# Optimization experiments

Hardware: AMD Instinct MI355X
Metric: run time of the kernel (lower is better)

Reference implementation:

```python
import jax, jax.numpy as jnp
import numpy as np

HIDDEN = 4096
NUM_HEADS = 32
NUM_KV_HEADS = 8
HEAD_DIM = 128
ROPE_THETA = 10000.0


def setup_inputs() -> dict:
    key = jax.random.key(0)
    ks = jax.random.split(key, 5)
    B, N = 2, 2048
    s = 0.02
    return {
        "hidden_states": jax.random.normal(ks[0], (B, N, HIDDEN), dtype=jnp.float32),
        "positions": jnp.tile(jnp.arange(N, dtype=jnp.int32)[None, :], (B, 1)),
        "Wq": jax.random.normal(ks[1], (HIDDEN, NUM_HEADS * HEAD_DIM), dtype=jnp.float32) * s,
        "Wk": jax.random.normal(ks[2], (HIDDEN, NUM_KV_HEADS * HEAD_DIM), dtype=jnp.float32) * s,
        "Wv": jax.random.normal(ks[3], (HIDDEN, NUM_KV_HEADS * HEAD_DIM), dtype=jnp.float32) * s,
        "Wo": jax.random.normal(ks[4], (NUM_HEADS * HEAD_DIM, HIDDEN), dtype=jnp.float32) * s,
    }


def _rotate_half(x):
    half = x.shape[-1] // 2
    return jnp.concatenate([-x[..., half:], x[..., :half]], axis=-1)


def reference(hidden_states, positions, Wq, Wk, Wv, Wo):
    B, N, _ = hidden_states.shape
    H, KVH, D = NUM_HEADS, NUM_KV_HEADS, HEAD_DIM
    rep = H // KVH

    # projections
    q = (hidden_states @ Wq).reshape(B, N, H, D).transpose(0, 2, 1, 3)     # [B,H,N,D]
    k = (hidden_states @ Wk).reshape(B, N, KVH, D).transpose(0, 2, 1, 3)   # [B,KVH,N,D]
    v = (hidden_states @ Wv).reshape(B, N, KVH, D).transpose(0, 2, 1, 3)   # [B,KVH,N,D]

    # rotary embedding
    inv_freq = 1.0 / (ROPE_THETA ** (jnp.arange(0, D, 2, dtype=jnp.float32) / D))
    freqs = positions.astype(jnp.float32)[..., None] * inv_freq            # [B,N,D/2]
    emb = jnp.concatenate([freqs, freqs], axis=-1)                          # [B,N,D]
    cos = jnp.cos(emb)[:, None, :, :]                                       # [B,1,N,D]
    sin = jnp.sin(emb)[:, None, :, :]
    q = q * cos + _rotate_half(q) * sin
    k = k * cos + _rotate_half(k) * sin

    # GQA attention without materializing repeated k/v:
    # group q heads by kv head (repeat_interleave => q head h uses kv group h//rep)
    qg = q.reshape(B, KVH, rep, N, D)
    scale = 1.0 / jnp.sqrt(jnp.asarray(D, dtype=q.dtype))
    scores = jnp.einsum('bgrnd,bgmd->bgrnm', qg, k) * scale                 # [B,KVH,rep,N,N]
    causal = jnp.tril(jnp.ones((N, N), dtype=bool))
    scores = jnp.where(causal, scores, jnp.finfo(scores.dtype).min)
    attn = jax.nn.softmax(scores, axis=-1)
    out = jnp.einsum('bgrnm,bgmd->bgrnd', attn, v)                          # [B,KVH,rep,N,D]
    out = out.reshape(B, H, N, D).transpose(0, 2, 1, 3).reshape(B, N, H * D)
    return out @ Wo
```

## Files before the change

### kernel.cpp

```cpp
#include <hip/hip_runtime.h>
#include <hip/hip_bf16.h>

typedef __bf16 bf16_t;
typedef float  f32x4  __attribute__((ext_vector_type(4)));
typedef bf16_t bf16x2 __attribute__((ext_vector_type(2)));
typedef bf16_t bf16x4 __attribute__((ext_vector_type(4)));
typedef bf16_t bf16x8 __attribute__((ext_vector_type(8)));

#define MFMA16(a, b, c) __builtin_amdgcn_mfma_f32_16x16x32_bf16((a), (b), (c), 0, 0, 0)

#define GLOAD_LDS16(g, l)                                                              \
  __builtin_amdgcn_global_load_lds((const __attribute__((address_space(1))) void*)(g), \
                                   (__attribute__((address_space(3))) void*)(l), 16, 0, 0)

#define BARRIER    __builtin_amdgcn_s_barrier()
#define WAIT_LGKM0 asm volatile("s_waitcnt lgkmcnt(0)" ::: "memory")
#define WAIT_LGKM8 asm volatile("s_waitcnt lgkmcnt(8)" ::: "memory")
#define WAIT_VM3   asm volatile("s_waitcnt vmcnt(3)" ::: "memory")
#define WAIT_VM4   asm volatile("s_waitcnt vmcnt(4)" ::: "memory")
#define WAIT_VM0   asm volatile("s_waitcnt vmcnt(0)" ::: "memory")

__global__ __launch_bounds__(256) void cvt_bf16(const float* __restrict__ in,
                                                bf16_t* __restrict__ out, int n4) {
  int stride = gridDim.x * blockDim.x;
  for (int i = blockIdx.x * blockDim.x + threadIdx.x; i < n4; i += stride) {
    f32x4 v = ((const f32x4*)in)[i];
    bf16x4 o;
#pragma unroll
    for (int j = 0; j < 4; ++j) o[j] = (bf16_t)v[j];
    ((bf16x4*)out)[i] = o;
  }
}

__global__ __launch_bounds__(256) void transpose_cvt(const float* __restrict__ in,
                                                     bf16_t* __restrict__ out,
                                                     int R, int C) {
  __shared__ float t[64][65];
  int tr0 = blockIdx.y * 64, tc0 = blockIdx.x * 64;
  int tx = threadIdx.x & 15, ty = threadIdx.x >> 4;
#pragma unroll
  for (int i = 0; i < 4; ++i) {
    f32x4 v = *(const f32x4*)(in + (size_t)(tr0 + ty + 16 * i) * C + tc0 + tx * 4);
#pragma unroll
    for (int j = 0; j < 4; ++j) t[ty + 16 * i][tx * 4 + j] = v[j];
  }
  __syncthreads();
#pragma unroll
  for (int i = 0; i < 4; ++i) {
    bf16x4 o4;
#pragma unroll
    for (int j = 0; j < 4; ++j) o4[j] = (bf16_t)t[tx * 4 + j][ty + 16 * i];
    *(bf16x4*)(out + (size_t)(tc0 + ty + 16 * i) * R + tr0 + tx * 4) = o4;
  }
}

#define LDB8(bf)                                                                         \
  {                                                                                      \
    const int sb_ = bBase0 + (bf)*16384;                                                 \
    _Pragma("unroll") for (int nf = 0; nf < 4; ++nf) {                                   \
      int row_ = brow0 + nf * 16 + ci;                                                   \
      _Pragma("unroll") for (int ks = 0; ks < 2; ++ks)                                   \
          b[nf][ks] = *(const bf16x8*)&lds[sb_ + row_ * 64 + ((ks * 32 + g * 8) ^ co)];  \
    }                                                                                    \
  }

#define LDA4(bf, q)                                                                      \
  {                                                                                      \
    const int sb_ = aBase0 + (bf)*16384;                                                 \
    _Pragma("unroll") for (int j = 0; j < 2; ++j) {                                      \
      int row_ = ((q)*2 + j) * 16 + ci;                                                  \
      _Pragma("unroll") for (int ks = 0; ks < 2; ++ks)                                   \
          a[j][ks] = *(const bf16x8*)&lds[sb_ + row_ * 64 + ((ks * 32 + g * 8) ^ co)];   \
    }                                                                                    \
  }

#define MMQ(q)                                                                           \
  {                                                                                      \
    __builtin_amdgcn_s_setprio(1);                                                       \
    _Pragma("unroll") for (int j = 0; j < 2; ++j)                                        \
        _Pragma("unroll") for (int nf = 0; nf < 4; ++nf)                                 \
            _Pragma("unroll") for (int ks = 0; ks < 2; ++ks)                             \
                acc[(q)*2 + j][nf] = MFMA16(a[j][ks], b[nf][ks], acc[(q)*2 + j][nf]);    \
    __builtin_amdgcn_s_setprio(0);                                                       \
  }

template <int WRITE_BF16>
__global__ __launch_bounds__(512) void gemm8o(const bf16_t* __restrict__ A,
                                              const bf16_t* __restrict__ Bt,
                                              void* __restrict__ Cv,
                                              int N, int K, int ntn) {
  __shared__ alignas(16) bf16_t lds[65536];
  const int tid = threadIdx.x;
  const int lane = tid & 63, w = tid >> 6;
  const int wr = w >> 2, wc = w & 3;
  const int g = lane >> 4, ci = lane & 15;
  const int cpx = gridDim.x >> 3;
  const int wg = ((int)blockIdx.x & 7) * cpx + ((int)blockIdx.x >> 3);
  const int m0 = (wg / ntn) * 256, n0 = (wg % ntn) * 256;
  const int ksw = ((lane & 7) ^ (lane >> 3)) << 3;
  const int aBase0 = wr * 8192;
  const int bBase0 = 32768 + (wc >> 1) * 8192;
  const int brow0 = (wc & 1) * 64;
  const int co = (ci & 7) << 3;

  const bf16_t* As[2] = {A + (size_t)m0 * K, A + (size_t)(m0 + 128) * K};
  const bf16_t* Bs[2] = {Bt + (size_t)n0 * K, Bt + (size_t)(n0 + 128) * K};

  auto stage = [&](const bf16_t* src, int kk, int ldsbase) {
#pragma unroll
    for (int j = 0; j < 2; ++j)
      GLOAD_LDS16(src + (size_t)(j * 64 + w * 8 + (lane >> 3)) * K + kk + ksw,
                  (char*)&lds[ldsbase + (j * 64 + w * 8) * 64]);
  };

  bf16x8 a[2][2], b[4][2];
  f32x4 acc[8][4];
#pragma unroll
  for (int mf = 0; mf < 8; ++mf)
#pragma unroll
    for (int nf = 0; nf < 4; ++nf) acc[mf][nf] = f32x4{0.f, 0.f, 0.f, 0.f};

  stage(As[0], 0, 0);
  stage(As[1], 0, 8192);
  stage(Bs[0], 0, 32768);
  stage(Bs[1], 0, 40960);
  stage(Bs[0], 64, 49152);
  stage(Bs[1], 64, 57344);
  WAIT_VM4;
  BARRIER;

  const int NT2 = K >> 7;
  for (int i = 0; i < NT2; ++i) {
    const int keb = i << 7;
    const int kA1 = keb + 64;
    int e2 = keb + 128;
    if (e2 > K - 64) e2 = K - 64;
    int o2 = keb + 192;
    if (o2 > K - 64) o2 = K - 64;
    LDA4(0, 0) LDB8(0)
    stage(As[0], kA1, 16384);
    WAIT_LGKM8;
    BARRIER; WAIT_LGKM0;
    MMQ(0)
    BARRIER;
    LDA4(0, 1)
    stage(As[1], kA1, 24576);
    BARRIER; WAIT_LGKM0;
    MMQ(1)
    BARRIER;
    LDA4(0, 2)
    stage(Bs[0], e2, 32768);
    BARRIER; WAIT_LGKM0;
    MMQ(2)
    BARRIER;
    LDA4(0, 3)
    stage(Bs[1], e2, 40960);
    BARRIER; WAIT_LGKM0;
    MMQ(3)
    WAIT_VM4;
    BARRIER;
    LDA4(1, 0) LDB8(1)
    stage(As[0], e2, 0);
    WAIT_LGKM8;
    BARRIER; WAIT_LGKM0;
    MMQ(0)
    BARRIER;
    LDA4(1, 1)
    stage(As[1], e2, 8192);
    BARRIER; WAIT_LGKM0;
    MMQ(1)
    BARRIER;
    LDA4(1, 2)
    stage(Bs[0], o2, 49152);
    BARRIER; WAIT_LGKM0;
    MMQ(2)
    BARRIER;
    LDA4(1, 3)
    stage(Bs[1], o2, 57344);
    BARRIER; WAIT_LGKM0;
    MMQ(3)
    WAIT_VM4;
    BARRIER;
  }
  WAIT_VM0;

#pragma unroll
  for (int mf = 0; mf < 8; ++mf) {
#pragma unroll
    for (int nf = 0; nf < 4; ++nf) {
      int grow = m0 + wr * 128 + mf * 16 + g * 4;
      int gcol = n0 + wc * 64 + nf * 16 + ci;
#pragma unroll
      for (int r = 0; r < 4; ++r) {
        if (WRITE_BF16)
          ((bf16_t*)Cv)[(size_t)(grow + r) * N + gcol] = (bf16_t)acc[mf][nf][r];
        else
          ((float*)Cv)[(size_t)(grow + r) * N + gcol] = acc[mf][nf][r];
      }
    }
  }
}

#define QLDB12(bf)                                                                        \
  {                                                                                       \
    const int sb_ = 32768 + (bf)*12288;                                                   \
    _Pragma("unroll") for (int nf = 0; nf < 6; ++nf) {                                    \
      int row_ = wc * 96 + nf * 16 + ci;                                                  \
      _Pragma("unroll") for (int ks = 0; ks < 2; ++ks)                                    \
          b[nf][ks] = *(const bf16x8*)&lds[sb_ + row_ * 64 + ((ks * 32 + g * 8) ^ co)];   \
    }                                                                                     \
  }

#define QLDA2(bf, q)                                                                      \
  {                                                                                       \
    const int sb_ = (bf)*16384;                                                           \
    const int row_ = wr * 64 + (q)*16 + ci;                                               \
    _Pragma("unroll") for (int ks = 0; ks < 2; ++ks)                                      \
        a[ks] = *(const bf16x8*)&lds[sb_ + row_ * 64 + ((ks * 32 + g * 8) ^ co)];         \
  }

#define QMMQ(q)                                                                           \
  {                                                                                       \
    __builtin_amdgcn_s_setprio(1);                                                        \
    _Pragma("unroll") for (int nf = 0; nf < 6; ++nf)                                      \
        _Pragma("unroll") for (int ks = 0; ks < 2; ++ks)                                  \
            acc[q][nf] = MFMA16(a[ks], b[nf][ks], acc[q][nf]);                            \
    __builtin_amdgcn_s_setprio(0);                                                        \
  }

__global__ __launch_bounds__(512) void gemm8qkv(const bf16_t* __restrict__ A,
                                                const bf16_t* __restrict__ Bt,
                                                bf16_t* __restrict__ C,
                                                int N, int K, int ntn) {
  __shared__ alignas(16) bf16_t lds[57344];
  const int tid = threadIdx.x;
  const int lane = tid & 63, w = tid >> 6;
  const int wr = w >> 1, wc = w & 1;
  const int g = lane >> 4, ci = lane & 15;
  const int cpx = gridDim.x >> 3;
  const int wg = ((int)blockIdx.x & 7) * cpx + ((int)blockIdx.x >> 3);
  const int m0 = (wg / ntn) * 256, n0 = (wg % ntn) * 192;
  const int ksw = ((lane & 7) ^ (lane >> 3)) << 3;
  const int co = (ci & 7) << 3;

  const bf16_t* Ar[4] = {A + (size_t)m0 * K, A + (size_t)(m0 + 64) * K,
                         A + (size_t)(m0 + 128) * K, A + (size_t)(m0 + 192) * K};
  const bf16_t* Br[3] = {Bt + (size_t)n0 * K, Bt + (size_t)(n0 + 64) * K,
                         Bt + (size_t)(n0 + 128) * K};

  auto stage64 = [&](const bf16_t* src, int kk, int ldsbase) {
    GLOAD_LDS16(src + (size_t)(w * 8 + (lane >> 3)) * K + kk + ksw,
                (char*)&lds[ldsbase + w * 512]);
  };

  bf16x8 a[2], b[6][2];
  f32x4 acc[4][6];
#pragma unroll
  for (int mf = 0; mf < 4; ++mf)
#pragma unroll
    for (int nf = 0; nf < 6; ++nf) acc[mf][nf] = f32x4{0.f, 0.f, 0.f, 0.f};

#pragma unroll
  for (int c = 0; c < 4; ++c) stage64(Ar[c], 0, c * 4096);
#pragma unroll
  for (int c = 0; c < 3; ++c) stage64(Br[c], 0, 32768 + c * 4096);
#pragma unroll
  for (int c = 0; c < 3; ++c) stage64(Br[c], 64, 45056 + c * 4096);
  WAIT_VM3;
  BARRIER;

  const int NT2 = K >> 7;
  for (int i = 0; i < NT2; ++i) {
    const int keb = i << 7;
    const int kA1 = keb + 64;
    int e2 = keb + 128;
    if (e2 > K - 64) e2 = K - 64;
    int o2 = keb + 192;
    if (o2 > K - 64) o2 = K - 64;
    QLDA2(0, 0) QLDB12(0)
    stage64(Ar[0], kA1, 16384);
    stage64(Ar[1], kA1, 16384 + 4096);
    WAIT_LGKM8;
    BARRIER; WAIT_LGKM0;
    QMMQ(0)
    BARRIER;
    QLDA2(0, 1)
    stage64(Ar[2], kA1, 16384 + 8192);
    stage64(Ar[3], kA1, 16384 + 12288);
    BARRIER; WAIT_LGKM0;
    QMMQ(1)
    BARRIER;
    QLDA2(0, 2)
    stage64(Br[0], e2, 32768);
    stage64(Br[1], e2, 32768 + 4096);
    BARRIER; WAIT_LGKM0;
    QMMQ(2)
    BARRIER;
    QLDA2(0, 3)
    stage64(Br[2], e2, 32768 + 8192);
    BARRIER; WAIT_LGKM0;
    QMMQ(3)
    WAIT_VM3;
    BARRIER;
    QLDA2(1, 0) QLDB12(1)
    stage64(Ar[0], e2, 0);
    stage64(Ar[1], e2, 4096);
    WAIT_LGKM8;
    BARRIER; WAIT_LGKM0;
    QMMQ(0)
    BARRIER;
    QLDA2(1, 1)
    stage64(Ar[2], e2, 8192);
    stage64(Ar[3], e2, 12288);
    BARRIER; WAIT_LGKM0;
    QMMQ(1)
    BARRIER;
    QLDA2(1, 2)
    stage64(Br[0], o2, 45056);
    stage64(Br[1], o2, 45056 + 4096);
    BARRIER; WAIT_LGKM0;
    QMMQ(2)
    BARRIER;
    QLDA2(1, 3)
    stage64(Br[2], o2, 45056 + 8192);
    BARRIER; WAIT_LGKM0;
    QMMQ(3)
    WAIT_VM3;
    BARRIER;
  }
  WAIT_VM0;

#pragma unroll
  for (int mf = 0; mf < 4; ++mf) {
#pragma unroll
    for (int nf = 0; nf < 6; ++nf) {
      int grow = m0 + wr * 64 + mf * 16 + g * 4;
      int gcol = n0 + wc * 96 + nf * 16 + ci;
#pragma unroll
      for (int r = 0; r < 4; ++r)
        C[(size_t)(grow + r) * N + gcol] = (bf16_t)acc[mf][nf][r];
    }
  }
}

__global__ __launch_bounds__(256) void rope_kv(const bf16_t* __restrict__ QKV,
                                               const int* __restrict__ pos,
                                               bf16_t* __restrict__ Kr,
                                               bf16_t* __restrict__ Vr) {
  int unit = blockIdx.x * 8 + (threadIdx.x >> 5);
  int l = threadIdx.x & 31;
  int token = unit >> 3, kvh = unit & 7;
  int b = token >> 11, n = token & 2047;
  const bf16_t* base = QKV + (size_t)token * 6144;
  {
    const bf16_t* src = base + 4096 + kvh * 128;
    bf16_t* dst = Kr + ((size_t)(b * 8 + kvh) * 2048 + n) * 128;
    float p = (float)pos[token];
    float a0 = p * exp2f(-(float)(2 * l) * 0.20762050593045702f);
    float a1 = p * exp2f(-(float)(2 * l + 1) * 0.20762050593045702f);
    float sn0, cs0, sn1, cs1;
    sincosf(a0, &sn0, &cs0);
    sincosf(a1, &sn1, &cs1);
    bf16x2 x0 = *(const bf16x2*)(src + 2 * l);
    bf16x2 x1 = *(const bf16x2*)(src + 64 + 2 * l);
    bf16x2 o0, o1;
    o0[0] = (bf16_t)((float)x0[0] * cs0 - (float)x1[0] * sn0);
    o0[1] = (bf16_t)((float)x0[1] * cs1 - (float)x1[1] * sn1);
    o1[0] = (bf16_t)((float)x1[0] * cs0 + (float)x0[0] * sn0);
    o1[1] = (bf16_t)((float)x1[1] * cs1 + (float)x0[1] * sn1);
    *(bf16x2*)(dst + 2 * l) = o0;
    *(bf16x2*)(dst + 64 + 2 * l) = o1;
  }
  {
    const bf16_t* src = base + 5120 + kvh * 128;
    bf16_t* dst = Vr + ((size_t)(b * 8 + kvh) * 2048 + n) * 128;
    *(bf16x4*)(dst + 4 * l) = *(const bf16x4*)(src + 4 * l);
  }
}

__global__ __launch_bounds__(512) void attn_kernel(const bf16_t* __restrict__ QKV,
                                                   const bf16_t* __restrict__ K,
                                                   const bf16_t* __restrict__ V,
                                                   const int* __restrict__ pos,
                                                   bf16_t* __restrict__ O) {
  const float scale2 = 0.12751743f;
  __shared__ alignas(16) bf16_t Kl[64 * 128];
  __shared__ alignas(16) bf16_t Vt[128 * 64];
  __shared__ alignas(16) bf16_t Pl[8][32 * 64];
  const int tid = threadIdx.x;
  const int lane = tid & 63, w = tid >> 6;
  const int g = lane >> 4, ci = lane & 15;
  const int hb = blockIdx.y;
  const int b = hb >> 5, h = hb & 31, kvh = h >> 2;
  const int p = blockIdx.x;
  const int qtB = 15 - p;
  const int qr[2] = {p * 128 + w * 16, qtB * 128 + w * 16};
  const bf16_t* Kh = K + (size_t)(b * 8 + kvh) * 2048 * 128;
  const bf16_t* Vh = V + (size_t)(b * 8 + kvh) * 2048 * 128;

  bf16x8 bq[2][4];
#pragma unroll
  for (int qb = 0; qb < 2; ++qb) {
    const int n = qr[qb] + ci;
    const bf16_t* qp = QKV + (size_t)(b * 2048 + n) * 6144 + h * 128;
    bf16x8 raw[4];
#pragma unroll
    for (int ks = 0; ks < 4; ++ks) raw[ks] = *(const bf16x8*)(qp + ks * 32 + g * 8);
    float ppos = (float)pos[b * 2048 + n];
#pragma unroll
    for (int k2 = 0; k2 < 2; ++k2)
#pragma unroll
      for (int j = 0; j < 8; ++j) {
        int d = k2 * 32 + g * 8 + j;
        float ang = ppos * exp2f(-(float)d * 0.20762050593045702f);
        float sn, cs;
        sincosf(ang, &sn, &cs);
        float x0 = (float)raw[k2][j], x1 = (float)raw[k2 + 2][j];
        bq[qb][k2][j] = (bf16_t)(x0 * cs - x1 * sn);
        bq[qb][k2 + 2][j] = (bf16_t)(x1 * cs + x0 * sn);
      }
  }

  f32x4 o[2][8];
#pragma unroll
  for (int qb = 0; qb < 2; ++qb)
#pragma unroll
    for (int nb = 0; nb < 8; ++nb) o[qb][nb] = f32x4{0.f, 0.f, 0.f, 0.f};
  float mrow[2] = {-1e30f, -1e30f};
  float lrow[2] = {0.f, 0.f};

  bf16x8 kreg[2];
  bf16x4 rv[4];
  const int kq = tid >> 5, dq = tid & 31;
  auto loadKV = [&](int kv0) {
#pragma unroll
    for (int i = 0; i < 2; ++i) {
      int c = tid + i * 512;
      kreg[i] = *(const bf16x8*)(Kh + (size_t)(kv0 + (c >> 4)) * 128 + (c & 15) * 8);
    }
#pragma unroll
    for (int rr = 0; rr < 4; ++rr)
      rv[rr] = *(const bf16x4*)(Vh + (size_t)(kv0 + kq * 4 + rr) * 128 + dq * 4);
  };
  auto writeKV = [&]() {
#pragma unroll
    for (int i = 0; i < 2; ++i) {
      int c = tid + i * 512;
      int row = c >> 4, kc = (c & 15) * 8;
      int sw = ((row ^ (row >> 3)) & 7) << 4;
      *(bf16x8*)((char*)Kl + row * 256 + ((kc * 2) ^ sw)) = kreg[i];
    }
#pragma unroll
    for (int jj = 0; jj < 4; ++jj) {
      int d = dq * 4 + jj;
      bf16x4 cv;
#pragma unroll
      for (int rr = 0; rr < 4; ++rr) cv[rr] = rv[rr][jj];
      int sw = ((d ^ (d >> 3)) & 7) << 4;
      *(bf16x4*)((char*)Vt + d * 128 + ((kq * 8) ^ sw)) = cv;
    }
  };

  const int nt = (qtB + 1) * 2;
  loadKV(0);
  for (int t = 0; t < nt; ++t) {
    const int kv0 = t * 64;
    __syncthreads();
    writeKV();
    __syncthreads();
    if (t + 1 < nt) loadKV(kv0 + 64);

    bool act[2] = {kv0 <= qr[0] + 15, kv0 <= qr[1] + 15};
#pragma unroll
    for (int qb = 0; qb < 2; ++qb) {
      if (!act[qb]) continue;
      f32x4 st[4];
#pragma unroll
      for (int kvb = 0; kvb < 4; ++kvb) st[kvb] = f32x4{0.f, 0.f, 0.f, 0.f};
      __builtin_amdgcn_s_setprio(1);
#pragma unroll
      for (int kvb = 0; kvb < 4; ++kvb) {
        int row = kvb * 16 + ci;
        int sw = ((row ^ (row >> 3)) & 7) << 4;
#pragma unroll
        for (int ks = 0; ks < 4; ++ks) {
          bf16x8 ak = *(const bf16x8*)((char*)Kl + row * 256 + ((ks * 64 + g * 16) ^ sw));
          st[kvb] = MFMA16(ak, bq[qb][ks], st[kvb]);
        }
      }
      __builtin_amdgcn_s_setprio(0);
      const int q = qr[qb] + ci;
      const bool needmask = (kv0 + 63 > qr[qb]);
      float pv[16];
      float pm = -1e30f;
#pragma unroll
      for (int kvb = 0; kvb < 4; ++kvb)
#pragma unroll
        for (int r = 0; r < 4; ++r) {
          float v = st[kvb][r] * scale2;
          if (needmask && (kv0 + kvb * 16 + 4 * g + r > q)) v = -1e30f;
          pv[kvb * 4 + r] = v;
          pm = fmaxf(pm, v);
        }
      pm = fmaxf(pm, __shfl_xor(pm, 16));
      pm = fmaxf(pm, __shfl_xor(pm, 32));
      const bool nskip = !__all((int)(pm <= mrow[qb] + 11.5f));
      const float mold = mrow[qb];
      float mnew = mold;
      float fs = 1.0f;
      if (nskip) {
        mnew = fmaxf(mold, pm);
        fs = exp2f(mold - mnew);
        mrow[qb] = mnew;
      }
      float ps = 0.f;
#pragma unroll
      for (int e = 0; e < 16; ++e) {
        pv[e] = exp2f(pv[e] - mnew);
        ps += pv[e];
      }
      ps += __shfl_xor(ps, 16);
      ps += __shfl_xor(ps, 32);
      lrow[qb] = (nskip ? lrow[qb] * fs : lrow[qb]) + ps;
      int prow = qb * 16 + ci;
      int swp = ((prow ^ (prow >> 3)) & 7) << 4;
#pragma unroll
      for (int kvb = 0; kvb < 4; ++kvb) {
        bf16x4 pk;
#pragma unroll
        for (int r = 0; r < 4; ++r) pk[r] = (bf16_t)pv[kvb * 4 + r];
        *(bf16x4*)((char*)&Pl[w][0] + prow * 128 + (((kvb * 16 + 4 * g) * 2) ^ swp)) = pk;
      }
      if (nskip) {
        float fo[4];
#pragma unroll
        for (int r = 0; r < 4; ++r) fo[r] = __shfl(fs, 4 * g + r);
#pragma unroll
        for (int nb = 0; nb < 8; ++nb)
#pragma unroll
          for (int r = 0; r < 4; ++r) o[qb][nb][r] *= fo[r];
      }
    }
    bf16x8 pa[2][2];
#pragma unroll
    for (int qb = 0; qb < 2; ++qb) {
      if (!act[qb]) continue;
      int prow = qb * 16 + ci;
      int swp = ((prow ^ (prow >> 3)) & 7) << 4;
#pragma unroll
      for (int ks = 0; ks < 2; ++ks)
        pa[qb][ks] = *(const bf16x8*)((char*)&Pl[w][0] + prow * 128 + ((ks * 64 + g * 16) ^ swp));
    }
    __builtin_amdgcn_s_setprio(1);
#pragma unroll
    for (int nb = 0; nb < 8; ++nb) {
      int d = nb * 16 + ci;
      int sw = ((d ^ (d >> 3)) & 7) << 4;
      bf16x8 bv0 = *(const bf16x8*)((char*)Vt + d * 128 + ((g * 16) ^ sw));
      bf16x8 bv1 = *(const bf16x8*)((char*)Vt + d * 128 + ((64 + g * 16) ^ sw));
#pragma unroll
      for (int qb = 0; qb < 2; ++qb) {
        if (!act[qb]) continue;
        o[qb][nb] = MFMA16(pa[qb][0], bv0, o[qb][nb]);
        o[qb][nb] = MFMA16(pa[qb][1], bv1, o[qb][nb]);
      }
    }
    __builtin_amdgcn_s_setprio(0);
  }
#pragma unroll
  for (int qb = 0; qb < 2; ++qb) {
    float linv = 1.0f / lrow[qb];
    float lv[4];
#pragma unroll
    for (int r = 0; r < 4; ++r) lv[r] = __shfl(linv, 4 * g + r);
#pragma unroll
    for (int r = 0; r < 4; ++r) {
      int n = qr[qb] + 4 * g + r;
      bf16_t* op = O + (size_t)(b * 2048 + n) * 4096 + h * 128;
#pragma unroll
      for (int nb = 0; nb < 8; ++nb) op[nb * 16 + ci] = (bf16_t)(o[qb][nb][r] * lv[r]);
    }
  }
}

extern "C" void kernel_launch(void* const* d_in, const int* in_sizes, int n_in,
                              void* d_out, int out_size, void* d_ws, size_t ws_size,
                              hipStream_t stream) {
  (void)in_sizes; (void)n_in; (void)out_size; (void)ws_size;
  const float* X = (const float*)d_in[0];
  const int* pos = (const int*)d_in[1];
  const float* Wq = (const float*)d_in[2];
  const float* Wk = (const float*)d_in[3];
  const float* Wv = (const float*)d_in[4];
  const float* Wo = (const float*)d_in[5];
  float* out = (float*)d_out;

  char* w = (char*)d_ws;
  auto carve = [&](size_t bytes) {
    void* p = (void*)w;
    w += (bytes + 255) & ~(size_t)255;
    return p;
  };
  const size_t T = 4096;
  bf16_t* Xbf    = (bf16_t*)carve(T * 4096 * 2);
  bf16_t* WqkvT  = (bf16_t*)carve(6144ull * 4096 * 2);
  bf16_t* WoT    = (bf16_t*)carve(4096ull * 4096 * 2);
  bf16_t* QKVraw = (bf16_t*)carve(T * 6144 * 2);
  bf16_t* Kr     = (bf16_t*)carve(T * 1024 * 2);
  bf16_t* Vr     = (bf16_t*)carve(T * 1024 * 2);
  bf16_t* Obf    = (bf16_t*)carve(T * 4096 * 2);

  cvt_bf16<<<2048, 256, 0, stream>>>(X, Xbf, (int)(T * 4096 / 4));
  transpose_cvt<<<dim3(64, 64), 256, 0, stream>>>(Wq, WqkvT, 4096, 4096);
  transpose_cvt<<<dim3(16, 64), 256, 0, stream>>>(Wk, WqkvT + 4096ull * 4096, 4096, 1024);
  transpose_cvt<<<dim3(16, 64), 256, 0, stream>>>(Wv, WqkvT + 5120ull * 4096, 4096, 1024);
  transpose_cvt<<<dim3(64, 64), 256, 0, stream>>>(Wo, WoT, 4096, 4096);

  gemm8qkv<<<512, 512, 0, stream>>>(Xbf, WqkvT, QKVraw, 6144, 4096, 32);

  rope_kv<<<(int)(T * 8 / 8), 256, 0, stream>>>(QKVraw, pos, Kr, Vr);

  attn_kernel<<<dim3(8, 64), 512, 0, stream>>>(QKVraw, Kr, Vr, pos, Obf);

  gemm8o<0><<<256, 512, 0, stream>>>(Obf, WoT, out, 4096, 4096, 16);
}
```

Before: 535.8 us.

## Enlarge attention KV tile to 128, load K via direct-to-LDS, merge weight transposes

The attention kernel now stages 128 keys per iteration instead of 64, which halves the number of barrier pairs. K is loaded with global_load_lds straight into swizzled shared memory, and the softmax scale is folded into Q at load time. P is written and read back per 64-key half within each wave, so the P buffer shrinks. The four weight transpose launches are merged into one kernel to cut launch overhead. In exchange the kernel uses more LDS, which may reduce occupancy, and the K load is no longer prefetched ahead of the barrier.

```diff
diff --git a/kernel.cpp b/kernel.cpp
--- a/kernel.cpp
+++ b/kernel.cpp
@@ -32,11 +32,31 @@
   }
 }
 
-__global__ __launch_bounds__(256) void transpose_cvt(const float* __restrict__ in,
-                                                     bf16_t* __restrict__ out,
-                                                     int R, int C) {
+__global__ __launch_bounds__(256) void transpose_all(const float* __restrict__ Wq,
+                                                     const float* __restrict__ Wk,
+                                                     const float* __restrict__ Wv,
+                                                     const float* __restrict__ Wo,
+                                                     bf16_t* __restrict__ WqkvT,
+                                                     bf16_t* __restrict__ WoT) {
   __shared__ float t[64][65];
-  int tr0 = blockIdx.y * 64, tc0 = blockIdx.x * 64;
+  const int bid = blockIdx.x;
+  const float* in;
+  bf16_t* out;
+  int C, cx, cy;
+  if (bid < 4096) {
+    in = Wq; out = WqkvT; C = 4096; cx = bid & 63; cy = bid >> 6;
+  } else if (bid < 5120) {
+    int tt = bid - 4096;
+    in = Wk; out = WqkvT + 4096ull * 4096; C = 1024; cx = tt & 15; cy = tt >> 4;
+  } else if (bid < 6144) {
+    int tt = bid - 5120;
+    in = Wv; out = WqkvT + 5120ull * 4096; C = 1024; cx = tt & 15; cy = tt >> 4;
+  } else {
+    int tt = bid - 6144;
+    in = Wo; out = WoT; C = 4096; cx = tt & 63; cy = tt >> 6;
+  }
+  const int R = 4096;
+  int tr0 = cy * 64, tc0 = cx * 64;
   int tx = threadIdx.x & 15, ty = threadIdx.x >> 4;
 #pragma unroll
   for (int i = 0; i < 4; ++i) {
@@ -384,9 +404,9 @@
                                                    const int* __restrict__ pos,
                                                    bf16_t* __restrict__ O) {
   const float scale2 = 0.12751743f;
-  __shared__ alignas(16) bf16_t Kl[64 * 128];
-  __shared__ alignas(16) bf16_t Vt[128 * 64];
-  __shared__ alignas(16) bf16_t Pl[8][32 * 64];
+  __shared__ alignas(16) bf16_t Kl[128 * 128];
+  __shared__ alignas(16) bf16_t Vt[128 * 128];
+  __shared__ alignas(16) bf16_t Pl[8][16 * 64];
   const int tid = threadIdx.x;
   const int lane = tid & 63, w = tid >> 6;
   const int g = lane >> 4, ci = lane & 15;
@@ -416,8 +436,8 @@
         float sn, cs;
         sincosf(ang, &sn, &cs);
         float x0 = (float)raw[k2][j], x1 = (float)raw[k2 + 2][j];
-        bq[qb][k2][j] = (bf16_t)(x0 * cs - x1 * sn);
-        bq[qb][k2 + 2][j] = (bf16_t)(x1 * cs + x0 * sn);
+        bq[qb][k2][j] = (bf16_t)((x0 * cs - x1 * sn) * scale2);
+        bq[qb][k2 + 2][j] = (bf16_t)((x1 * cs + x0 * sn) * scale2);
       }
   }
 
@@ -429,143 +449,133 @@
   float mrow[2] = {-1e30f, -1e30f};
   float lrow[2] = {0.f, 0.f};
 
-  bf16x8 kreg[2];
-  bf16x4 rv[4];
-  const int kq = tid >> 5, dq = tid & 31;
-  auto loadKV = [&](int kv0) {
-#pragma unroll
-    for (int i = 0; i < 2; ++i) {
+  bf16x4 rv[8];
+  const int kq2 = tid >> 5, dq = tid & 31;
+  auto loadV = [&](int kv0_) {
+#pragma unroll
+    for (int rr = 0; rr < 8; ++rr)
+      rv[rr] = *(const bf16x4*)(Vh + (size_t)(kv0_ + kq2 * 8 + rr) * 128 + dq * 4);
+  };
+
+  const int NT = qtB + 1;
+  const int swp = ((ci ^ (ci >> 3)) & 7) << 4;
+  loadV(0);
+  for (int it = 0; it < NT; ++it) {
+    const int kv0 = it * 128;
+    __syncthreads();
+#pragma unroll
+    for (int i = 0; i < 4; ++i) {
       int c = tid + i * 512;
-      kreg[i] = *(const bf16x8*)(Kh + (size_t)(kv0 + (c >> 4)) * 128 + (c & 15) * 8);
-    }
-#pragma unroll
-    for (int rr = 0; rr < 4; ++rr)
-      rv[rr] = *(const bf16x4*)(Vh + (size_t)(kv0 + kq * 4 + rr) * 128 + dq * 4);
-  };
-  auto writeKV = [&]() {
-#pragma unroll
-    for (int i = 0; i < 2; ++i) {
-      int c = tid + i * 512;
-      int row = c >> 4, kc = (c & 15) * 8;
-      int sw = ((row ^ (row >> 3)) & 7) << 4;
-      *(bf16x8*)((char*)Kl + row * 256 + ((kc * 2) ^ sw)) = kreg[i];
+      int row = c >> 4, gran = c & 15;
+      int gs = gran ^ ((row ^ (row >> 3)) & 7);
+      GLOAD_LDS16(Kh + (size_t)(kv0 + row) * 128 + gs * 8,
+                  (char*)Kl + i * 8192 + w * 1024);
     }
 #pragma unroll
     for (int jj = 0; jj < 4; ++jj) {
       int d = dq * 4 + jj;
-      bf16x4 cv;
-#pragma unroll
-      for (int rr = 0; rr < 4; ++rr) cv[rr] = rv[rr][jj];
+      bf16x8 cv;
+#pragma unroll
+      for (int rr = 0; rr < 8; ++rr) cv[rr] = rv[rr][jj];
       int sw = ((d ^ (d >> 3)) & 7) << 4;
-      *(bf16x4*)((char*)Vt + d * 128 + ((kq * 8) ^ sw)) = cv;
+      *(bf16x8*)((char*)Vt + d * 256 + ((kq2 * 16) ^ sw)) = cv;
     }
-  };
-
-  const int nt = (qtB + 1) * 2;
-  loadKV(0);
-  for (int t = 0; t < nt; ++t) {
-    const int kv0 = t * 64;
     __syncthreads();
-    writeKV();
-    __syncthreads();
-    if (t + 1 < nt) loadKV(kv0 + 64);
-
-    bool act[2] = {kv0 <= qr[0] + 15, kv0 <= qr[1] + 15};
-#pragma unroll
-    for (int qb = 0; qb < 2; ++qb) {
-      if (!act[qb]) continue;
-      f32x4 st[4];
-#pragma unroll
-      for (int kvb = 0; kvb < 4; ++kvb) st[kvb] = f32x4{0.f, 0.f, 0.f, 0.f};
+    if (it + 1 < NT) loadV(kv0 + 128);
+
+#pragma unroll
+    for (int hh = 0; hh < 2; ++hh) {
+      const int kvh0 = kv0 + hh * 64;
+      bool act[2] = {kvh0 <= qr[0] + 15, kvh0 <= qr[1] + 15};
+      bf16x8 pa[2][2];
+#pragma unroll
+      for (int qb = 0; qb < 2; ++qb) {
+        if (!act[qb]) continue;
+        f32x4 st[4];
+#pragma unroll
+        for (int kvb = 0; kvb < 4; ++kvb) st[kvb] = f32x4{0.f, 0.f, 0.f, 0.f};
+        __builtin_amdgcn_s_setprio(1);
+#pragma unroll
+        for (int kvb = 0; kvb < 4; ++kvb) {
+          int row = hh * 64 + kvb * 16 + ci;
+          int sw = ((row ^ (row >> 3)) & 7) << 4;
+#pragma unroll
+          for (int ks = 0; ks < 4; ++ks) {
+            bf16x8 ak = *(const bf16x8*)((char*)Kl + row * 256 + ((ks * 64 + g * 16) ^ sw));
+            st[kvb] = MFMA16(ak, bq[qb][ks], st[kvb]);
+          }
+        }
+        __builtin_amdgcn_s_setprio(0);
+        const int q = qr[qb] + ci;
+        const bool needmask = (kvh0 + 63 > qr[qb]);
+        float pm = -1e30f;
+#pragma unroll
+        for (int kvb = 0; kvb < 4; ++kvb)
+#pragma unroll
+          for (int r = 0; r < 4; ++r) {
+            float v = st[kvb][r];
+            if (needmask && (kvh0 + kvb * 16 + 4 * g + r > q)) v = -1e30f;
+            st[kvb][r] = v;
+            pm = fmaxf(pm, v);
+          }
+        pm = fmaxf(pm, __shfl_xor(pm, 16));
+        pm = fmaxf(pm, __shfl_xor(pm, 32));
+        const bool nskip = !__all((int)(pm <= mrow[qb] + 11.5f));
+        const float mold = mrow[qb];
+        float mnew = mold;
+        float fs = 1.0f;
+        if (nskip) {
+          mnew = fmaxf(mold, pm);
+          fs = exp2f(mold - mnew);
+          mrow[qb] = mnew;
+        }
+        float ps = 0.f;
+#pragma unroll
+        for (int kvb = 0; kvb < 4; ++kvb)
+#pragma unroll
+          for (int r = 0; r < 4; ++r) {
+            st[kvb][r] = exp2f(st[kvb][r] - mnew);
+            ps += st[kvb][r];
+          }
+        ps += __shfl_xor(ps, 16);
+        ps += __shfl_xor(ps, 32);
+        lrow[qb] = (nskip ? lrow[qb] * fs : lrow[qb]) + ps;
+#pragma unroll
+        for (int kvb = 0; kvb < 4; ++kvb) {
+          bf16x4 pk;
+#pragma unroll
+          for (int r = 0; r < 4; ++r) pk[r] = (bf16_t)st[kvb][r];
+          *(bf16x4*)((char*)&Pl[w][0] + ci * 128 + (((kvb * 16 + 4 * g) * 2) ^ swp)) = pk;
+        }
+#pragma unroll
+        for (int ks = 0; ks < 2; ++ks)
+          pa[qb][ks] = *(const bf16x8*)((char*)&Pl[w][0] + ci * 128 + ((ks * 64 + g * 16) ^ swp));
+        if (nskip) {
+          float fo[4];
+#pragma unroll
+          for (int r = 0; r < 4; ++r) fo[r] = __shfl(fs, 4 * g + r);
+#pragma unroll
+          for (int nb = 0; nb < 8; ++nb)
+#pragma unroll
+            for (int r = 0; r < 4; ++r) o[qb][nb][r] *= fo[r];
+        }
+      }
       __builtin_amdgcn_s_setprio(1);
 #pragma unroll
-      for (int kvb = 0; kvb < 4; ++kvb) {
-        int row = kvb * 16 + ci;
-        int sw = ((row ^ (row >> 3)) & 7) << 4;
-#pragma unroll
-        for (int ks = 0; ks < 4; ++ks) {
-          bf16x8 ak = *(const bf16x8*)((char*)Kl + row * 256 + ((ks * 64 + g * 16) ^ sw));
-          st[kvb] = MFMA16(ak, bq[qb][ks], st[kvb]);
+      for (int nb = 0; nb < 8; ++nb) {
+        int d = nb * 16 + ci;
+        int sw = ((d ^ (d >> 3)) & 7) << 4;
+        bf16x8 bv0 = *(const bf16x8*)((char*)Vt + d * 256 + ((hh * 128 + g * 16) ^ sw));
+        bf16x8 bv1 = *(const bf16x8*)((char*)Vt + d * 256 + ((hh * 128 + 64 + g * 16) ^ sw));
+#pragma unroll
+        for (int qb = 0; qb < 2; ++qb) {
+          if (!act[qb]) continue;
+          o[qb][nb] = MFMA16(pa[qb][0], bv0, o[qb][nb]);
+          o[qb][nb] = MFMA16(pa[qb][1], bv1, o[qb][nb]);
         }
       }
       __builtin_amdgcn_s_setprio(0);
-      const int q = qr[qb] + ci;
-      const bool needmask = (kv0 + 63 > qr[qb]);
-      float pv[16];
-      float pm = -1e30f;
-#pragma unroll
-      for (int kvb = 0; kvb < 4; ++kvb)
-#pragma unroll
-        for (int r = 0; r < 4; ++r) {
-          float v = st[kvb][r] * scale2;
-          if (needmask && (kv0 + kvb * 16 + 4 * g + r > q)) v = -1e30f;
-          pv[kvb * 4 + r] = v;
-          pm = fmaxf(pm, v);
-        }
-      pm = fmaxf(pm, __shfl_xor(pm, 16));
-      pm = fmaxf(pm, __shfl_xor(pm, 32));
-      const bool nskip = !__all((int)(pm <= mrow[qb] + 11.5f));
-      const float mold = mrow[qb];
-      float mnew = mold;
-      float fs = 1.0f;
-      if (nskip) {
-        mnew = fmaxf(mold, pm);
-        fs = exp2f(mold - mnew);
-        mrow[qb] = mnew;
-      }
-      float ps = 0.f;
-#pragma unroll
-      for (int e = 0; e < 16; ++e) {
-        pv[e] = exp2f(pv[e] - mnew);
-        ps += pv[e];
-      }
-      ps += __shfl_xor(ps, 16);
-      ps += __shfl_xor(ps, 32);
-      lrow[qb] = (nskip ? lrow[qb] * fs : lrow[qb]) + ps;
-      int prow = qb * 16 + ci;
-      int swp = ((prow ^ (prow >> 3)) & 7) << 4;
-#pragma unroll
-      for (int kvb = 0; kvb < 4; ++kvb) {
-        bf16x4 pk;
-#pragma unroll
-        for (int r = 0; r < 4; ++r) pk[r] = (bf16_t)pv[kvb * 4 + r];
-        *(bf16x4*)((char*)&Pl[w][0] + prow * 128 + (((kvb * 16 + 4 * g) * 2) ^ swp)) = pk;
-      }
-      if (nskip) {
-        float fo[4];
-#pragma unroll
-        for (int r = 0; r < 4; ++r) fo[r] = __shfl(fs, 4 * g + r);
-#pragma unroll
-        for (int nb = 0; nb < 8; ++nb)
-#pragma unroll
-          for (int r = 0; r < 4; ++r) o[qb][nb][r] *= fo[r];
-      }
     }
-    bf16x8 pa[2][2];
-#pragma unroll
-    for (int qb = 0; qb < 2; ++qb) {
-      if (!act[qb]) continue;
-      int prow = qb * 16 + ci;
-      int swp = ((prow ^ (prow >> 3)) & 7) << 4;
-#pragma unroll
-      for (int ks = 0; ks < 2; ++ks)
-        pa[qb][ks] = *(const bf16x8*)((char*)&Pl[w][0] + prow * 128 + ((ks * 64 + g * 16) ^ swp));
-    }
-    __builtin_amdgcn_s_setprio(1);
-#pragma unroll
-    for (int nb = 0; nb < 8; ++nb) {
-      int d = nb * 16 + ci;
-      int sw = ((d ^ (d >> 3)) & 7) << 4;
-      bf16x8 bv0 = *(const bf16x8*)((char*)Vt + d * 128 + ((g * 16) ^ sw));
-      bf16x8 bv1 = *(const bf16x8*)((char*)Vt + d * 128 + ((64 + g * 16) ^ sw));
-#pragma unroll
-      for (int qb = 0; qb < 2; ++qb) {
-        if (!act[qb]) continue;
-        o[qb][nb] = MFMA16(pa[qb][0], bv0, o[qb][nb]);
-        o[qb][nb] = MFMA16(pa[qb][1], bv1, o[qb][nb]);
-      }
-    }
-    __builtin_amdgcn_s_setprio(0);
   }
 #pragma unroll
   for (int qb = 0; qb < 2; ++qb) {
@@ -611,10 +621,7 @@
   bf16_t* Obf    = (bf16_t*)carve(T * 4096 * 2);
 
   cvt_bf16<<<2048, 256, 0, stream>>>(X, Xbf, (int)(T * 4096 / 4));
-  transpose_cvt<<<dim3(64, 64), 256, 0, stream>>>(Wq, WqkvT, 4096, 4096);
-  transpose_cvt<<<dim3(16, 64), 256, 0, stream>>>(Wk, WqkvT + 4096ull * 4096, 4096, 1024);
-  transpose_cvt<<<dim3(16, 64), 256, 0, stream>>>(Wv, WqkvT + 5120ull * 4096, 4096, 1024);
-  transpose_cvt<<<dim3(64, 64), 256, 0, stream>>>(Wo, WoT, 4096, 4096);
+  transpose_all<<<10240, 256, 0, stream>>>(Wq, Wk, Wv, Wo, WqkvT, WoT);
 
   gemm8qkv<<<512, 512, 0, stream>>>(Xbf, WqkvT, QKVraw, 6144, 4096, 32);
 
```

Measured after the change: 560.5 us. +4.6%, slower.
